# Kernel tuning notes

Hardware: AMD Instinct MI355X
Metric: run time of the kernel (lower is better)

Reference implementation:

```python
import jax, jax.numpy as jnp
import numpy as np

K_RADIUS = 1            # 2k+1 = 3 neighborhood -> 9 offsets
AFF_THRESH = 0.5        # affinity = 1/(1+dist); edge iff affinity > 0.5 (dist < 1)
N_PROP_STEPS = 40       # label propagation iterations
M_PARENTS = 256         # max parent segments per image (num_nodes of next level)


def _offsets(k):
    return [(dy, dx) for dy in range(-k, k + 1) for dx in range(-k, k + 1)]


def _shift2d(x, dy, dx, fill):
    """Shift spatial dims (axes 1,2) of x by (dy,dx), padding with `fill`."""
    kr = K_RADIUS
    pad = [(0, 0), (kr, kr), (kr, kr)] + [(0, 0)] * (x.ndim - 3)
    xp = jnp.pad(x, pad, constant_values=fill)
    H, W = x.shape[1], x.shape[2]
    return xp[:, kr + dy:kr + dy + H, kr + dx:kr + dx + W]


def setup_inputs() -> dict:
    key = jax.random.key(0)
    features = jax.random.normal(key, (32, 128, 128, 64), dtype=jnp.float32)
    return {"features": features}


def reference(features):
    BT, H, W, C = features.shape
    N = H * W
    offs = _offsets(K_RADIUS)

    # ---- compute_affinities: inverse Euclidean distance in (2k+1)^2 window ----
    aff_list = []
    for dy, dx in offs:
        nb = _shift2d(features, dy, dx, fill=1e6)  # out-of-bounds -> huge dist -> aff ~ 0
        dist = jnp.sqrt(jnp.sum((features - nb) ** 2, axis=-1) + 1e-12)
        aff_list.append(1.0 / (1.0 + dist))
    affinities = jnp.stack(aff_list, axis=-1)      # [BT,H,W,K]

    # ---- threshold_affinities ----
    edges = affinities > AFF_THRESH                # [BT,H,W,K] bool

    # ---- compute_parents: label propagation (min-label flooding over edges) ----
    labels0 = jnp.broadcast_to(
        jnp.arange(N, dtype=jnp.int32).reshape(1, H, W), (BT, H, W))
    SENT = jnp.int32(N)  # sentinel larger than any label

    def body(_, lab):
        cands = [lab]
        for j, (dy, dx) in enumerate(offs):
            nb = _shift2d(lab, dy, dx, fill=N)
            cands.append(jnp.where(edges[..., j], nb, SENT))
        return jnp.min(jnp.stack(cands, axis=0), axis=0)

    labels = jax.lax.fori_loop(0, N_PROP_STEPS, body, labels0)  # [BT,H,W]
    lab_flat = labels.reshape(BT, N)

    # ---- register_parents: relabel to contiguous ids, capped at M (preproc_segment_ids) ----
    def relabel(lab):
        present = jnp.zeros((N,), jnp.int32).at[lab].set(1)
        rank = jnp.cumsum(present) - 1
        return jnp.minimum(rank[lab], M_PARENTS - 1)

    seg = jax.vmap(relabel)(lab_flat)              # [BT,N] in [0,M)

    # ---- aggregate_nodes_and_features: per-segment mean and variance ----
    flat_ids = (seg + jnp.arange(BT, dtype=jnp.int32)[:, None] * M_PARENTS).reshape(-1)
    feat = features.reshape(BT * N, C)
    sums = jax.ops.segment_sum(feat, flat_ids, num_segments=BT * M_PARENTS)
    sqs = jax.ops.segment_sum(feat * feat, flat_ids, num_segments=BT * M_PARENTS)
    cnt = jax.ops.segment_sum(jnp.ones((BT * N, 1), feat.dtype), flat_ids,
                              num_segments=BT * M_PARENTS)
    denom = jnp.maximum(cnt, 1.0)
    mean = sums / denom
    var = jnp.maximum(sqs / denom - mean * mean, 0.0)
    parent_nodes = jnp.concatenate([mean, var], axis=-1).reshape(BT, M_PARENTS, 2 * C)
    return parent_nodes
```

## Files before the change

### kernel.cpp

```cpp
#include <hip/hip_runtime.h>
#include <stdint.h>

#define HH 128
#define WW 128
#define NPIX 16384
#define BTN 32
#define CCH 64
#define MPAR 256
#define SENT 16384
#define NSTEPS 40

#define ETX 32
#define ETY 8
__global__ __launch_bounds__(256) void edge_kernel(const float* __restrict__ feat,
                                                   unsigned char* __restrict__ mask4,
                                                   float4* __restrict__ accz,
                                                   float4* __restrict__ cntz) {
  __shared__ float lds[8][308];
  int blk = blockIdx.x;
  int tid = threadIdx.x;

  if (tid < 128) accz[blk * 128 + tid] = make_float4(0.f, 0.f, 0.f, 0.f);
  else if (tid == 128) cntz[blk] = make_float4(0.f, 0.f, 0.f, 0.f);

  int b = blk >> 6;
  int t = blk & 63;
  int ty0 = (t >> 2) * ETY;
  int tx0 = (t & 3) * ETX;
  const float* fb = feat + ((size_t)b << 20);

  for (int sp = tid; sp < 306; sp += 256) {
    int gy = ty0 + sp / 34;
    int gx = tx0 - 1 + sp % 34;
    if (gy < HH && (unsigned)gx < (unsigned)WW) {
      const float* pp = fb + (((size_t)(gy << 7) + gx) << 6);
      float4 v0 = *(const float4*)pp;
      float4 v1 = *(const float4*)(pp + 4);
      lds[0][sp] = v0.x; lds[1][sp] = v0.y; lds[2][sp] = v0.z; lds[3][sp] = v0.w;
      lds[4][sp] = v1.x; lds[5][sp] = v1.y; lds[6][sp] = v1.z; lds[7][sp] = v1.w;
    } else {
#pragma unroll
      for (int c = 0; c < 8; ++c) lds[c][sp] = 1e6f;
    }
  }
  __syncthreads();

  int tx = tid & 31, ty = tid >> 5;
  int idx = ty * 34 + tx + 1;
  int gx = tx0 + tx, gy = ty0 + ty;

  float own[8];
#pragma unroll
  for (int c = 0; c < 8; ++c) own[c] = lds[c][idx];
  float a0 = 0.f, a1 = 0.f, a2 = 0.f, a3 = 0.f;
#pragma unroll
  for (int c = 0; c < 8; ++c) {
    float o = own[c];
    float d0 = o - lds[c][idx + 1];
    float d1 = o - lds[c][idx + 33];
    float d2 = o - lds[c][idx + 34];
    float d3 = o - lds[c][idx + 35];
    a0 += d0 * d0; a1 += d1 * d1; a2 += d2 * d2; a3 += d3 * d3;
  }

  bool vS = (gy + 1) < HH;
  float acc[4] = {a0, a1, a2, a3};
  bool val[4] = {(gx + 1) < WW, vS && gx >= 1, vS, vS && (gx + 1) < WW};
  const int offp[4] = {1, 127, 128, 129};
  const float* fp = fb + (((size_t)(gy << 7) + gx) << 6);
  unsigned m = 0;
#pragma unroll
  for (int j = 0; j < 4; ++j) {
    if (val[j]) {
      float s = acc[j];
      if (s < 1.0f) {
        const float* np_ = fp + ((size_t)offp[j] << 6);
        for (int c = 8; c < 64; ++c) {
          float d = fp[c] - np_[c];
          s += d * d;
        }
      }
      if (s + 1e-12f < 1.0f) m |= (1u << j);
    }
  }
  mask4[(b << 14) + (gy << 7) + gx] = (unsigned char)m;
}

__global__ __launch_bounds__(1024) void prop_kernel(const unsigned char* __restrict__ mask4g,
                                                    unsigned char* __restrict__ segg) {
  __shared__ __align__(16) unsigned short lab[NPIX];
  __shared__ __align__(16) unsigned char e8[NPIX];
  __shared__ __align__(16) unsigned short rnk[NPIX];
  __shared__ int flags[2];
  __shared__ int wsum[16];
  __shared__ int wexc[16];
  int b = blockIdx.x;
  int tid = threadIdx.x;
  int lane = tid & 63, wid = tid >> 6;

  ((uint4*)e8)[tid] = ((const uint4*)(mask4g + ((size_t)b << 14)))[tid];
  __syncthreads();

  unsigned char tmp[16];
  {
    int base = tid * 16;
#pragma unroll
    for (int i = 0; i < 16; ++i) {
      int p = base + i;
      int y = p >> 7, x = p & (WW - 1);
      unsigned own = e8[p];
      unsigned nw = (y > 0 && x > 0) ? e8[p - 129] : 0;
      unsigned n_ = (y > 0) ? e8[p - 128] : 0;
      unsigned ne = (y > 0 && x < WW - 1) ? e8[p - 127] : 0;
      unsigned w_ = (x > 0) ? e8[p - 1] : 0;
      unsigned v = ((nw >> 3) & 1) | (((n_ >> 2) & 1) << 1) | (((ne >> 1) & 1) << 2) |
                   ((w_ & 1) << 3) | ((own & 1) << 4) | (((own >> 1) & 1) << 5) |
                   (((own >> 2) & 1) << 6) | (((own >> 3) & 1) << 7);
      tmp[i] = (unsigned char)v;
    }
  }
  __syncthreads();
  {
    int base = tid * 16;
#pragma unroll
    for (int i = 0; i < 16; ++i) e8[base + i] = tmp[i];
#pragma unroll
    for (int i = 0; i < 16; ++i) lab[base + i] = (unsigned short)(base + i);
  }
  if (tid == 0) { flags[0] = 0; flags[1] = 0; }
  __syncthreads();

  int x0 = (tid & 31) * 4, y0 = (tid >> 5) * 4;
  int cur[4][4], eb[4][4];
#pragma unroll
  for (int r = 0; r < 4; ++r)
#pragma unroll
    for (int c = 0; c < 4; ++c) {
      cur[r][c] = (y0 + r) * WW + x0 + c;
      eb[r][c] = e8[(y0 + r) * WW + x0 + c];
    }

  for (int it = 0; it < NSTEPS; ++it) {
    int top[6], bot[6], lft[4], rgt[4];
#pragma unroll
    for (int c = 0; c < 6; ++c) {
      top[c] = lab[(((y0 - 1) * WW) + x0 - 1 + c) & (NPIX - 1)];
      bot[c] = lab[(((y0 + 4) * WW) + x0 - 1 + c) & (NPIX - 1)];
    }
#pragma unroll
    for (int r = 0; r < 4; ++r) {
      lft[r] = lab[(((y0 + r) * WW) + x0 - 1) & (NPIX - 1)];
      rgt[r] = lab[(((y0 + r) * WW) + x0 + 4) & (NPIX - 1)];
    }
    int nl[4][4];
    bool ch = false;
#pragma unroll
    for (int r = 0; r < 4; ++r) {
#pragma unroll
      for (int c = 0; c < 4; ++c) {
        int m = cur[r][c];
        int e = eb[r][c];
        int v;
        v = (r > 0) ? ((c > 0) ? cur[r - 1][c - 1] : lft[r - 1]) : top[c];
        m = min(m, (e & 1) ? v : SENT);
        v = (r > 0) ? cur[r - 1][c] : top[c + 1];
        m = min(m, (e & 2) ? v : SENT);
        v = (r > 0) ? ((c < 3) ? cur[r - 1][c + 1] : rgt[r - 1]) : top[c + 2];
        m = min(m, (e & 4) ? v : SENT);
        v = (c > 0) ? cur[r][c - 1] : lft[r];
        m = min(m, (e & 8) ? v : SENT);
        v = (c < 3) ? cur[r][c + 1] : rgt[r];
        m = min(m, (e & 16) ? v : SENT);
        v = (r < 3) ? ((c > 0) ? cur[r + 1][c - 1] : lft[r + 1]) : bot[c];
        m = min(m, (e & 32) ? v : SENT);
        v = (r < 3) ? cur[r + 1][c] : bot[c + 1];
        m = min(m, (e & 64) ? v : SENT);
        v = (r < 3) ? ((c < 3) ? cur[r + 1][c + 1] : rgt[r + 1]) : bot[c + 2];
        m = min(m, (e & 128) ? v : SENT);
        nl[r][c] = m;
        ch |= (m != cur[r][c]);
      }
    }
    __syncthreads();
#pragma unroll
    for (int r = 0; r < 4; ++r) {
      unsigned lo = (unsigned)nl[r][0] | ((unsigned)nl[r][1] << 16);
      unsigned hi = (unsigned)nl[r][2] | ((unsigned)nl[r][3] << 16);
      *((uint2*)&lab[(y0 + r) * WW + x0]) = make_uint2(lo, hi);
    }
    if (ch) flags[it & 1] = 1;
    if (tid == 0) flags[(it + 1) & 1] = 0;
#pragma unroll
    for (int r = 0; r < 4; ++r)
#pragma unroll
      for (int c = 0; c < 4; ++c) cur[r][c] = nl[r][c];
    __syncthreads();
    if (!flags[it & 1]) break;
  }

  __syncthreads();
  ((uint4*)e8)[tid] = make_uint4(0u, 0u, 0u, 0u);
  __syncthreads();
#pragma unroll
  for (int i = 0; i < 16; ++i) {
    int p = tid + i * 1024;
    e8[lab[p]] = 1;
  }
  __syncthreads();
  int pres[16];
  int base = tid * 16;
#pragma unroll
  for (int i = 0; i < 16; ++i) pres[i] = e8[base + i];
  int s_local = 0;
#pragma unroll
  for (int i = 0; i < 16; ++i) s_local += pres[i];
  int inc = s_local;
#pragma unroll
  for (int off = 1; off < 64; off <<= 1) {
    int v = __shfl_up(inc, off, 64);
    if (lane >= off) inc += v;
  }
  if (lane == 63) wsum[wid] = inc;
  __syncthreads();
  if (wid == 0) {
    int tt = (lane < 16) ? wsum[lane] : 0;
    int winc = tt;
#pragma unroll
    for (int off = 1; off < 16; off <<= 1) {
      int v = __shfl_up(winc, off, 64);
      if (lane >= off) winc += v;
    }
    if (lane < 16) wexc[lane] = winc - tt;
  }
  __syncthreads();
  int run = wexc[wid] + (inc - s_local);
#pragma unroll
  for (int i = 0; i < 16; ++i) {
    run += pres[i];
    rnk[base + i] = (unsigned short)(run - 1);
  }
  __syncthreads();
  unsigned char* so = segg + ((size_t)b << 14);
#pragma unroll
  for (int i = 0; i < 16; ++i) {
    int p = tid + i * 1024;
    int sg = rnk[lab[p]];
    so[p] = (unsigned char)min(sg, 255);
  }
}

#define PXW 128
__global__ __launch_bounds__(256) void agg_kernel(const float* __restrict__ feat,
                                                  const unsigned char* __restrict__ segg,
                                                  float* __restrict__ acc,
                                                  float* __restrict__ cnt) {
  int lane = threadIdx.x & 63;
  int gw = blockIdx.x * 4 + (threadIdx.x >> 6);
  int b = gw >> 7;
  int chunk = gw & 127;
  int basep = (b << 14) + (chunk << 7);
  const unsigned char* sp = segg + basep;
  int s0 = sp[lane];
  int s1 = sp[64 + lane];
  const float* fp = feat + ((size_t)basep << 6) + lane;

  float sacc = 0.f, qacc = 0.f, cacc = 0.f;
  int curs = __builtin_amdgcn_readlane(s0, 0);

  float v[32];
#pragma unroll
  for (int u = 0; u < 32; ++u) v[u] = fp[(size_t)u << 6];

#pragma unroll
  for (int kk = 0; kk < PXW; kk += 32) {
    float w[32];
    if (kk + 32 < PXW) {
#pragma unroll
      for (int u = 0; u < 32; ++u) w[u] = fp[(size_t)(kk + 32 + u) << 6];
    }
#pragma unroll
    for (int u = 0; u < 32; ++u) {
      int k = kk + u;
      int sg = __builtin_amdgcn_readlane((k & 64) ? s1 : s0, k & 63);
      if (sg != curs) {
        float* a = acc + ((size_t)((b << 8) + curs) << 7);
        atomicAdd(a + lane, sacc);
        atomicAdd(a + 64 + lane, qacc);
        if (lane == 0) atomicAdd(cnt + (b << 8) + curs, cacc);
        curs = sg; sacc = 0.f; qacc = 0.f; cacc = 0.f;
      }
      sacc += v[u]; qacc += v[u] * v[u]; cacc += 1.f;
    }
#pragma unroll
    for (int u = 0; u < 32; ++u) v[u] = w[u];
  }
  {
    float* a = acc + ((size_t)((b << 8) + curs) << 7);
    atomicAdd(a + lane, sacc);
    atomicAdd(a + 64 + lane, qacc);
    if (lane == 0) atomicAdd(cnt + (b << 8) + curs, cacc);
  }
}

__global__ __launch_bounds__(256) void fin_kernel(float* __restrict__ acc,
                                                  const float* __restrict__ cnt) {
  int gid = blockIdx.x * 256 + threadIdx.x;
  int bm = gid >> 6, c = gid & 63;
  float* a = acc + ((size_t)bm << 7);
  float s = a[c], q = a[c + 64];
  float n = cnt[bm];
  float denom = fmaxf(n, 1.0f);
  float mean = s / denom;
  float var = fmaxf(q / denom - mean * mean, 0.0f);
  a[c] = mean;
  a[c + 64] = var;
}

extern "C" void kernel_launch(void* const* d_in, const int* in_sizes, int n_in,
                              void* d_out, int out_size, void* d_ws, size_t ws_size,
                              hipStream_t stream) {
  const float* feat = (const float*)d_in[0];
  unsigned char* mask4 = (unsigned char*)d_ws;
  unsigned char* segg = mask4 + (size_t)BTN * NPIX;
  float* cnt = (float*)(segg + (size_t)BTN * NPIX);
  float* acc = (float*)d_out;

  edge_kernel<<<BTN * 64, 256, 0, stream>>>(feat, mask4, (float4*)acc, (float4*)cnt);
  prop_kernel<<<BTN, 1024, 0, stream>>>(mask4, segg);
  agg_kernel<<<BTN * NPIX / PXW / 4, 256, 0, stream>>>(feat, segg, acc, cnt);
  fin_kernel<<<BTN * MPAR * CCH / 256, 256, 0, stream>>>(acc, cnt);
}
```

Baseline: 229.0 us.

## Split aggregation wave into two pixel streams with float2 loads

The aggregation kernel now assigns 64 pixels per wave instead of 128 and doubles the grid. Each half-wave handles alternating pixels, loading two channels per lane as float2, so one wave processes two pixel streams at once. Each stream tracks its own run of segment ids and flushes partial sums with atomics when the segment changes. This roughly halves the serial per-wave loop length and widens the loads. In exchange it can issue more atomics, because runs are split across the two streams and across more chunks.

```diff
diff --git a/kernel.cpp b/kernel.cpp
--- a/kernel.cpp
+++ b/kernel.cpp
@@ -249,56 +249,68 @@
   }
 }
 
-#define PXW 128
+#define CHK 64
 __global__ __launch_bounds__(256) void agg_kernel(const float* __restrict__ feat,
                                                   const unsigned char* __restrict__ segg,
                                                   float* __restrict__ acc,
                                                   float* __restrict__ cnt) {
   int lane = threadIdx.x & 63;
   int gw = blockIdx.x * 4 + (threadIdx.x >> 6);
-  int b = gw >> 7;
-  int chunk = gw & 127;
-  int basep = (b << 14) + (chunk << 7);
-  const unsigned char* sp = segg + basep;
-  int s0 = sp[lane];
-  int s1 = sp[64 + lane];
-  const float* fp = feat + ((size_t)basep << 6) + lane;
-
-  float sacc = 0.f, qacc = 0.f, cacc = 0.f;
-  int curs = __builtin_amdgcn_readlane(s0, 0);
-
-  float v[32];
-#pragma unroll
-  for (int u = 0; u < 32; ++u) v[u] = fp[(size_t)u << 6];
-
-#pragma unroll
-  for (int kk = 0; kk < PXW; kk += 32) {
-    float w[32];
-    if (kk + 32 < PXW) {
-#pragma unroll
-      for (int u = 0; u < 32; ++u) w[u] = fp[(size_t)(kk + 32 + u) << 6];
-    }
-#pragma unroll
-    for (int u = 0; u < 32; ++u) {
-      int k = kk + u;
-      int sg = __builtin_amdgcn_readlane((k & 64) ? s1 : s0, k & 63);
-      if (sg != curs) {
-        float* a = acc + ((size_t)((b << 8) + curs) << 7);
-        atomicAdd(a + lane, sacc);
-        atomicAdd(a + 64 + lane, qacc);
-        if (lane == 0) atomicAdd(cnt + (b << 8) + curs, cacc);
-        curs = sg; sacc = 0.f; qacc = 0.f; cacc = 0.f;
+  int b = gw >> 8;
+  int chunk = gw & 255;
+  int basep = (b << 14) + (chunk << 6);
+  int s0 = segg[basep + lane];
+  const float2* fp2 = (const float2*)(feat + ((size_t)basep << 6));
+
+  float2 v[32];
+#pragma unroll
+  for (int k = 0; k < 32; ++k) v[k] = fp2[(k << 6) + lane];
+
+  int half = lane >> 5;
+  int c0 = (lane & 31) << 1;
+  int rowb = (b << 8);
+  float sx = 0.f, sy = 0.f, qx = 0.f, qy = 0.f;
+  float cA = 0.f, cB = 0.f;
+  int cursA = __builtin_amdgcn_readlane(s0, 0);
+  int cursB = __builtin_amdgcn_readlane(s0, 1);
+
+#pragma unroll
+  for (int k = 0; k < 32; ++k) {
+    int sgA = __builtin_amdgcn_readlane(s0, 2 * k);
+    int sgB = __builtin_amdgcn_readlane(s0, 2 * k + 1);
+    if (sgA != cursA) {
+      if (half == 0) {
+        float* a = acc + ((size_t)(rowb + cursA) << 7) + c0;
+        atomicAdd(a, sx); atomicAdd(a + 1, sy);
+        atomicAdd(a + 64, qx); atomicAdd(a + 65, qy);
+        if (lane == 0) atomicAdd(cnt + rowb + cursA, cA);
+        sx = 0.f; sy = 0.f; qx = 0.f; qy = 0.f;
       }
-      sacc += v[u]; qacc += v[u] * v[u]; cacc += 1.f;
-    }
-#pragma unroll
-    for (int u = 0; u < 32; ++u) v[u] = w[u];
+      cA = 0.f;
+      cursA = sgA;
+    }
+    if (sgB != cursB) {
+      if (half == 1) {
+        float* a = acc + ((size_t)(rowb + cursB) << 7) + c0;
+        atomicAdd(a, sx); atomicAdd(a + 1, sy);
+        atomicAdd(a + 64, qx); atomicAdd(a + 65, qy);
+        if (lane == 32) atomicAdd(cnt + rowb + cursB, cB);
+        sx = 0.f; sy = 0.f; qx = 0.f; qy = 0.f;
+      }
+      cB = 0.f;
+      cursB = sgB;
+    }
+    sx += v[k].x; sy += v[k].y;
+    qx += v[k].x * v[k].x; qy += v[k].y * v[k].y;
+    cA += 1.f; cB += 1.f;
   }
   {
-    float* a = acc + ((size_t)((b << 8) + curs) << 7);
-    atomicAdd(a + lane, sacc);
-    atomicAdd(a + 64 + lane, qacc);
-    if (lane == 0) atomicAdd(cnt + (b << 8) + curs, cacc);
+    int crs = half ? cursB : cursA;
+    float* a = acc + ((size_t)(rowb + crs) << 7) + c0;
+    atomicAdd(a, sx); atomicAdd(a + 1, sy);
+    atomicAdd(a + 64, qx); atomicAdd(a + 65, qy);
+    if (lane == 0) atomicAdd(cnt + rowb + cursA, cA);
+    if (lane == 32) atomicAdd(cnt + rowb + cursB, cB);
   }
 }
 
@@ -327,6 +339,6 @@
 
   edge_kernel<<<BTN * 64, 256, 0, stream>>>(feat, mask4, (float4*)acc, (float4*)cnt);
   prop_kernel<<<BTN, 1024, 0, stream>>>(mask4, segg);
-  agg_kernel<<<BTN * NPIX / PXW / 4, 256, 0, stream>>>(feat, segg, acc, cnt);
+  agg_kernel<<<BTN * NPIX / CHK / 4, 256, 0, stream>>>(feat, segg, acc, cnt);
   fin_kernel<<<BTN * MPAR * CCH / 256, 256, 0, stream>>>(acc, cnt);
 }
```

New measurement: 329.6 us. +43.9%, slower.
